# Optimization experiments

Measured on AMD Instinct MI355X. Metric: run time of the kernel, lower is better.

## Reference

```python
import jax, jax.numpy as jnp
import numpy as np

T, D, E, K, F = 512, 2048, 64, 8, 768  # tokens, hidden, experts, top_k, moe_intermediate

def setup_inputs() -> dict:
    key = jax.random.key(0)
    k0, k1, k2, k3, k4 = jax.random.split(key, 5)
    std = 0.02
    return {
        "hidden_states": jax.random.normal(k0, (T, D), dtype=jnp.float32),
        "gate_w": jax.random.normal(k1, (D, E), dtype=jnp.float32) * std,
        "w_gate": jax.random.normal(k2, (E, D, F), dtype=jnp.float32) * std,  # per-expert gate proj
        "w_up":   jax.random.normal(k3, (E, D, F), dtype=jnp.float32) * std,  # per-expert up proj
        "w_down": jax.random.normal(k4, (E, F, D), dtype=jnp.float32) * std,  # per-expert down proj
    }

def reference(hidden_states, gate_w, w_gate, w_up, w_down):
    x = hidden_states  # [T, D]
    # Router: gate linear -> softmax -> top-k -> renormalize (norm_topk_prob=True)
    router_logits = x @ gate_w                      # [T, E]
    probs = jax.nn.softmax(router_logits, axis=-1)  # [T, E]
    topk_w, topk_idx = jax.lax.top_k(probs, K)      # [T, K]
    topk_w = topk_w / jnp.sum(topk_w, axis=-1, keepdims=True)
    # Combine weights as dense [T, E] scatter (zero for unrouted experts)
    cw = jnp.zeros((T, E), dtype=x.dtype).at[jnp.arange(T)[:, None], topk_idx].set(topk_w)
    # Experts: SwiGLU MLP per expert, dense dispatch then weighted combine
    g = jnp.einsum('td,edf->etf', x, w_gate)        # [E, T, F]
    u = jnp.einsum('td,edf->etf', x, w_up)          # [E, T, F]
    h = jax.nn.silu(g) * u                          # [E, T, F]
    y = jnp.einsum('etf,efd->etd', h, w_down)       # [E, T, D]
    out = jnp.einsum('te,etd->td', cw, y)           # [T, D]
    return out
```

## Files before the change

### kernel.cpp

```cpp
#include <hip/hip_runtime.h>
#include <hip/hip_bf16.h>

#define T_TOK 512
#define D_DIM 2048
#define E_NUM 64
#define K_TOP 8
#define F_DIM 768

typedef __bf16 bf16x8 __attribute__((ext_vector_type(8)));
typedef float  f32x4  __attribute__((ext_vector_type(4)));

#define AS1 __attribute__((address_space(1)))
#define AS3 __attribute__((address_space(3)))

__device__ __forceinline__ void gll16(const void* g, void* l) {
    __builtin_amdgcn_global_load_lds((const AS1 uint32_t*)g, (AS3 uint32_t*)l, 16, 0, 0);
}

#define VM_WAIT_I(N) asm volatile("s_waitcnt vmcnt(" #N ")" ::: "memory")
#define VM_WAIT(N) VM_WAIT_I(N)

#define PIPE_STEP(WN, BUF, DOSTG, KN)            \
    do {                                          \
        VM_WAIT(WN);                              \
        __builtin_amdgcn_sched_barrier(0);        \
        __builtin_amdgcn_s_barrier();             \
        consume(BUF);                             \
        __builtin_amdgcn_s_barrier();             \
        __builtin_amdgcn_sched_barrier(0);        \
        if (DOSTG) stage(BUF, KN);                \
    } while (0)

#define WS_IDS   4096
#define WS_PW    139264
#define WS_XBF   155648
#define WS_H     2252800
#define WS_Y     8544256

__global__ void zero_cnt_kernel(int* __restrict__ cnt) {
    if (threadIdx.x < E_NUM) cnt[threadIdx.x] = 0;
}

__global__ __launch_bounds__(256) void xcvt_kernel(
        const float* __restrict__ x, __bf16* __restrict__ xb) {
    const size_t i = ((size_t)blockIdx.x * 256 + threadIdx.x) * 8;
    const float4 a = *(const float4*)(x + i);
    const float4 b = *(const float4*)(x + i + 4);
    bf16x8 v;
    v[0]=(__bf16)a.x; v[1]=(__bf16)a.y; v[2]=(__bf16)a.z; v[3]=(__bf16)a.w;
    v[4]=(__bf16)b.x; v[5]=(__bf16)b.y; v[6]=(__bf16)b.z; v[7]=(__bf16)b.w;
    *(uint4*)(xb + i) = __builtin_bit_cast(uint4, v);
}

__global__ __launch_bounds__(256) void router_kernel(
        const float* __restrict__ x, const float* __restrict__ gw,
        float* __restrict__ pair_w, int* __restrict__ cnt, int* __restrict__ ids) {
    const int t   = blockIdx.x;
    const int tid = threadIdx.x;
    const int c   = tid >> 4;
    const int g   = tid & 15;

    const float* xr  = x + (size_t)t * D_DIM + c * 128;
    const float4* gr = (const float4*)(gw + (size_t)(c * 128) * E_NUM + g * 4);

    f32x4 acc; acc[0]=0.f; acc[1]=0.f; acc[2]=0.f; acc[3]=0.f;
    #pragma unroll 8
    for (int k = 0; k < 128; k++) {
        const float xv = xr[k];
        const float4 wv = gr[(size_t)k * 16];
        acc[0] += xv * wv.x; acc[1] += xv * wv.y;
        acc[2] += xv * wv.z; acc[3] += xv * wv.w;
    }
    __shared__ f32x4 part[16][16];
    part[c][g] = acc;
    __syncthreads();
    if (tid < 64) {
        const int e = tid;
        float logit = 0.f;
        #pragma unroll
        for (int cc = 0; cc < 16; cc++) logit += part[cc][e >> 2][e & 3];
        float cur = logit;
        float selV[8]; int selE[8];
        #pragma unroll
        for (int i = 0; i < 8; i++) {
            float bv = cur; int bi = e;
            #pragma unroll
            for (int off = 32; off > 0; off >>= 1) {
                float ov = __shfl_xor(bv, off);
                int   oi = __shfl_xor(bi, off);
                if (ov > bv || (ov == bv && oi < bi)) { bv = ov; bi = oi; }
            }
            selV[i] = bv; selE[i] = bi;
            if (e == bi) cur = -INFINITY;
        }
        const float m = selV[0];
        float sum = 0.f;
        #pragma unroll
        for (int i = 0; i < 8; i++) sum += __expf(selV[i] - m);
        float myW = 0.f; int myE = 0;
        #pragma unroll
        for (int i = 0; i < 8; i++) {
            if (e == i) { myW = __expf(selV[i] - m) / sum; myE = selE[i]; }
        }
        if (e < 8) {
            pair_w[t * K_TOP + e] = myW;
            int pos = atomicAdd(&cnt[myE], 1);
            ids[myE * T_TOK + pos] = t * K_TOP + e;
        }
    }
}

template<int NK, int BSTR, int MODE>
__global__ __launch_bounds__(256, 3) void gemm2_kernel(
        const __bf16* __restrict__ Abase, const float* __restrict__ B0w,
        const float* __restrict__ B1w, const int* __restrict__ cnt,
        const int* __restrict__ ids, __bf16* __restrict__ Out) {
    constexpr int NCT = (MODE == 0) ? (BSTR / 64) : (BSTR / 128);
    constexpr int NWG = NCT * E_NUM;
    constexpr int CHK = NWG / 8;
    const int bid = blockIdx.y * NCT + blockIdx.x;
    const int wg  = (bid & 7) * CHK + (bid >> 3);
    const int e   = wg / NCT;
    const int ct  = wg % NCT;
    const int n = cnt[e];
    if (n <= 0) return;

    const int tid  = threadIdx.x;
    const int lane = tid & 63;
    const int w    = tid >> 6;
    const int g16  = lane >> 4;
    const int l16  = lane & 15;

    __shared__ __align__(16) char lds[2][24576];

    const int bcol0 = (MODE == 0) ? ct * 64 : ct * 128;
    const int bcol1 = (MODE == 0) ? ct * 64 : ct * 128 + 64;
    const float* b0 = B0w + (size_t)e * NK * 32 * BSTR
                    + (size_t)(tid >> 4) * BSTR + bcol0 + (tid & 15) * 4;
    const float* b1 = B1w + (size_t)e * NK * 32 * BSTR
                    + (size_t)(tid >> 4) * BSTR + bcol1 + (tid & 15) * 4;
    const int ach = tid >> 7;
    const int arw = tid & 127;
    const int ci  = w * 16 + l16;

    for (int mt = 0; mt * 128 < n; mt++) {
        const int ap  = mt * 128 + arw;
        const int aid = ids[(size_t)e * T_TOK + (ap < n ? ap : n - 1)];
        const __bf16* asrc = Abase + (size_t)(MODE == 0 ? (aid >> 3) : aid)
                                   * (MODE == 0 ? D_DIM : F_DIM);

        f32x4 acc0[8], acc1[8];
        #pragma unroll
        for (int m = 0; m < 8; m++) {
            acc0[m][0]=0.f; acc0[m][1]=0.f; acc0[m][2]=0.f; acc0[m][3]=0.f;
            acc1[m][0]=0.f; acc1[m][1]=0.f; acc1[m][2]=0.f; acc1[m][3]=0.f;
        }

        auto stage = [&](int buf, int ks) {
            char* L = lds[buf];
            gll16(asrc + ks * 32 + ach * 8,        L + ach * 2048 + arw * 16);
            gll16(asrc + ks * 32 + (ach + 2) * 8,  L + (ach + 2) * 2048 + arw * 16);
            gll16(b0 + (size_t)(ks * 32) * BSTR,      L + 8192 + tid * 16);
            gll16(b0 + (size_t)(ks * 32 + 16) * BSTR, L + 8192 + 4096 + tid * 16);
            gll16(b1 + (size_t)(ks * 32) * BSTR,      L + 16384 + tid * 16);
            gll16(b1 + (size_t)(ks * 32 + 16) * BSTR, L + 16384 + 4096 + tid * 16);
        };
        auto consume = [&](int buf) {
            const char* L = lds[buf];
            const float* B0f = (const float*)(L + 8192);
            const float* B1f = (const float*)(L + 16384);
            bf16x8 bf0, bf1;
            #pragma unroll
            for (int i = 0; i < 8; i++) {
                bf0[i] = (__bf16)B0f[(g16 * 8 + i) * 64 + ci];
                bf1[i] = (__bf16)B1f[(g16 * 8 + i) * 64 + ci];
            }
            __builtin_amdgcn_s_setprio(1);
            #pragma unroll
            for (int m = 0; m < 8; m++) {
                bf16x8 af = __builtin_bit_cast(bf16x8,
                    *(const uint4*)(L + g16 * 2048 + (m * 16 + l16) * 16));
                acc0[m] = __builtin_amdgcn_mfma_f32_16x16x32_bf16(af, bf0, acc0[m], 0, 0, 0);
                acc1[m] = __builtin_amdgcn_mfma_f32_16x16x32_bf16(af, bf1, acc1[m], 0, 0, 0);
            }
            __builtin_amdgcn_s_setprio(0);
        };

        stage(0, 0); stage(1, 1);

        for (int ks = 0; ks < NK - 2; ks++) {
            PIPE_STEP(6, ks & 1, true, ks + 2);
        }
        PIPE_STEP(6, NK & 1, false, 0);
        PIPE_STEP(0, (NK - 1) & 1, false, 0);

        #pragma unroll
        for (int m = 0; m < 8; m++) {
            #pragma unroll
            for (int r = 0; r < 4; r++) {
                const int p = mt * 128 + m * 16 + g16 * 4 + r;
                if (p < n) {
                    const int rid = ids[(size_t)e * T_TOK + p];
                    if (MODE == 0) {
                        const float g = acc0[m][r], u = acc1[m][r];
                        const float hv = (g / (1.f + __expf(-g))) * u;
                        Out[(size_t)rid * F_DIM + ct * 64 + ci] = (__bf16)hv;
                    } else {
                        Out[(size_t)rid * D_DIM + ct * 128 + ci]      = (__bf16)acc0[m][r];
                        Out[(size_t)rid * D_DIM + ct * 128 + 64 + ci] = (__bf16)acc1[m][r];
                    }
                }
            }
        }
    }
}

__global__ __launch_bounds__(256) void combine_kernel(
        const __bf16* __restrict__ Y, const float* __restrict__ pw,
        float* __restrict__ out) {
    const int t   = blockIdx.x;
    const int tid = threadIdx.x;
    const int d0  = tid * 8;
    float acc[8];
    #pragma unroll
    for (int j = 0; j < 8; j++) acc[j] = 0.f;
    #pragma unroll
    for (int k = 0; k < K_TOP; k++) {
        const float wgt = pw[t * K_TOP + k];
        bf16x8 v = *(const bf16x8*)(Y + (size_t)(t * K_TOP + k) * D_DIM + d0);
        #pragma unroll
        for (int j = 0; j < 8; j++) acc[j] += wgt * (float)v[j];
    }
    #pragma unroll
    for (int j = 0; j < 8; j++) out[(size_t)t * D_DIM + d0 + j] = acc[j];
}

extern "C" void kernel_launch(void* const* d_in, const int* in_sizes, int n_in,
                              void* d_out, int out_size, void* d_ws, size_t ws_size,
                              hipStream_t stream) {
    const float* x      = (const float*)d_in[0];
    const float* gw     = (const float*)d_in[1];
    const float* w_gate = (const float*)d_in[2];
    const float* w_up   = (const float*)d_in[3];
    const float* w_down = (const float*)d_in[4];
    float* out = (float*)d_out;

    char* ws = (char*)d_ws;
    int*    cnt = (int*)(ws);
    int*    ids = (int*)(ws + WS_IDS);
    float*  pw  = (float*)(ws + WS_PW);
    __bf16* xbf = (__bf16*)(ws + WS_XBF);
    __bf16* H   = (__bf16*)(ws + WS_H);
    __bf16* Y   = (__bf16*)(ws + WS_Y);

    zero_cnt_kernel<<<1, 64, 0, stream>>>(cnt);
    xcvt_kernel<<<T_TOK * D_DIM / (256 * 8), 256, 0, stream>>>(x, xbf);
    router_kernel<<<T_TOK, 256, 0, stream>>>(x, gw, pw, cnt, ids);
    gemm2_kernel<64, F_DIM, 0><<<dim3(F_DIM / 64, E_NUM), 256, 0, stream>>>(
        xbf, w_gate, w_up, cnt, ids, H);
    gemm2_kernel<24, D_DIM, 1><<<dim3(D_DIM / 128, E_NUM), 256, 0, stream>>>(
        H, w_down, w_down, cnt, ids, Y);
    combine_kernel<<<T_TOK, 256, 0, stream>>>(Y, pw, out);
}
```

Measured before the change: 303.8 us.

## Load gathered A rows directly to registers and triple-buffer B tiles in LDS

The gathered activation (A) operand is no longer staged through LDS. Each lane loads its MFMA A fragment straight from global memory into registers, with two register sets alternating across k-steps. The B weight tiles now use three LDS buffers of 16 KB each instead of two of 24 KB, so each block allocates less LDS and prefetches one step further ahead. This is meant to hide memory latency better and cut LDS traffic, at the cost of more VGPRs and uncoalesced 16-byte global gathers per lane.

```diff
diff --git a/kernel.cpp b/kernel.cpp
--- a/kernel.cpp
+++ b/kernel.cpp
@@ -19,17 +19,8 @@
 
 #define VM_WAIT_I(N) asm volatile("s_waitcnt vmcnt(" #N ")" ::: "memory")
 #define VM_WAIT(N) VM_WAIT_I(N)
-
-#define PIPE_STEP(WN, BUF, DOSTG, KN)            \
-    do {                                          \
-        VM_WAIT(WN);                              \
-        __builtin_amdgcn_sched_barrier(0);        \
-        __builtin_amdgcn_s_barrier();             \
-        consume(BUF);                             \
-        __builtin_amdgcn_s_barrier();             \
-        __builtin_amdgcn_sched_barrier(0);        \
-        if (DOSTG) stage(BUF, KN);                \
-    } while (0)
+#define SB0() __builtin_amdgcn_sched_barrier(0)
+#define BAR() __builtin_amdgcn_s_barrier()
 
 #define WS_IDS   4096
 #define WS_PW    139264
@@ -112,10 +103,11 @@
 
 template<int NK, int BSTR, int MODE>
 __global__ __launch_bounds__(256, 3) void gemm2_kernel(
-        const __bf16* __restrict__ Abase, const float* __restrict__ B0w,
+        const char* __restrict__ Abase, const float* __restrict__ B0w,
         const float* __restrict__ B1w, const int* __restrict__ cnt,
         const int* __restrict__ ids, __bf16* __restrict__ Out) {
-    constexpr int NCT = (MODE == 0) ? (BSTR / 64) : (BSTR / 128);
+    constexpr int NCT   = (MODE == 0) ? (BSTR / 64) : (BSTR / 128);
+    constexpr int ASTRB = (MODE == 0) ? (D_DIM * 2) : (F_DIM * 2);
     constexpr int NWG = NCT * E_NUM;
     constexpr int CHK = NWG / 8;
     const int bid = blockIdx.y * NCT + blockIdx.x;
@@ -131,7 +123,7 @@
     const int g16  = lane >> 4;
     const int l16  = lane & 15;
 
-    __shared__ __align__(16) char lds[2][24576];
+    __shared__ __align__(16) char lds[3][16384];
 
     const int bcol0 = (MODE == 0) ? ct * 64 : ct * 128;
     const int bcol1 = (MODE == 0) ? ct * 64 : ct * 128 + 64;
@@ -139,15 +131,18 @@
                     + (size_t)(tid >> 4) * BSTR + bcol0 + (tid & 15) * 4;
     const float* b1 = B1w + (size_t)e * NK * 32 * BSTR
                     + (size_t)(tid >> 4) * BSTR + bcol1 + (tid & 15) * 4;
-    const int ach = tid >> 7;
-    const int arw = tid & 127;
-    const int ci  = w * 16 + l16;
+    const int ci = w * 16 + l16;
 
     for (int mt = 0; mt * 128 < n; mt++) {
-        const int ap  = mt * 128 + arw;
-        const int aid = ids[(size_t)e * T_TOK + (ap < n ? ap : n - 1)];
-        const __bf16* asrc = Abase + (size_t)(MODE == 0 ? (aid >> 3) : aid)
-                                   * (MODE == 0 ? D_DIM : F_DIM);
+        uint32_t aoff[8];
+        #pragma unroll
+        for (int m = 0; m < 8; m++) {
+            int p = mt * 128 + m * 16 + l16;
+            if (p >= n) p = n - 1;
+            const int aid = ids[(size_t)e * T_TOK + p];
+            const int row = (MODE == 0) ? (aid >> 3) : aid;
+            aoff[m] = (uint32_t)row * ASTRB + g16 * 16;
+        }
 
         f32x4 acc0[8], acc1[8];
         #pragma unroll
@@ -155,20 +150,24 @@
             acc0[m][0]=0.f; acc0[m][1]=0.f; acc0[m][2]=0.f; acc0[m][3]=0.f;
             acc1[m][0]=0.f; acc1[m][1]=0.f; acc1[m][2]=0.f; acc1[m][3]=0.f;
         }
+        uint4 sA[8], sB[8];
 
         auto stage = [&](int buf, int ks) {
             char* L = lds[buf];
-            gll16(asrc + ks * 32 + ach * 8,        L + ach * 2048 + arw * 16);
-            gll16(asrc + ks * 32 + (ach + 2) * 8,  L + (ach + 2) * 2048 + arw * 16);
-            gll16(b0 + (size_t)(ks * 32) * BSTR,      L + 8192 + tid * 16);
-            gll16(b0 + (size_t)(ks * 32 + 16) * BSTR, L + 8192 + 4096 + tid * 16);
-            gll16(b1 + (size_t)(ks * 32) * BSTR,      L + 16384 + tid * 16);
-            gll16(b1 + (size_t)(ks * 32 + 16) * BSTR, L + 16384 + 4096 + tid * 16);
+            gll16(b0 + (size_t)(ks * 32) * BSTR,      L + tid * 16);
+            gll16(b0 + (size_t)(ks * 32 + 16) * BSTR, L + 4096 + tid * 16);
+            gll16(b1 + (size_t)(ks * 32) * BSTR,      L + 8192 + tid * 16);
+            gll16(b1 + (size_t)(ks * 32 + 16) * BSTR, L + 12288 + tid * 16);
         };
-        auto consume = [&](int buf) {
+        auto loadA = [&](uint4 (&s)[8], int ks) {
+            #pragma unroll
+            for (int m = 0; m < 8; m++)
+                s[m] = *(const uint4*)(Abase + aoff[m] + ks * 64);
+        };
+        auto consume = [&](int buf, const uint4 (&s)[8]) {
             const char* L = lds[buf];
-            const float* B0f = (const float*)(L + 8192);
-            const float* B1f = (const float*)(L + 16384);
+            const float* B0f = (const float*)L;
+            const float* B1f = (const float*)(L + 8192);
             bf16x8 bf0, bf1;
             #pragma unroll
             for (int i = 0; i < 8; i++) {
@@ -178,21 +177,44 @@
             __builtin_amdgcn_s_setprio(1);
             #pragma unroll
             for (int m = 0; m < 8; m++) {
-                bf16x8 af = __builtin_bit_cast(bf16x8,
-                    *(const uint4*)(L + g16 * 2048 + (m * 16 + l16) * 16));
+                const bf16x8 af = __builtin_bit_cast(bf16x8, s[m]);
                 acc0[m] = __builtin_amdgcn_mfma_f32_16x16x32_bf16(af, bf0, acc0[m], 0, 0, 0);
                 acc1[m] = __builtin_amdgcn_mfma_f32_16x16x32_bf16(af, bf1, acc1[m], 0, 0, 0);
             }
             __builtin_amdgcn_s_setprio(0);
         };
 
-        stage(0, 0); stage(1, 1);
-
-        for (int ks = 0; ks < NK - 2; ks++) {
-            PIPE_STEP(6, ks & 1, true, ks + 2);
-        }
-        PIPE_STEP(6, NK & 1, false, 0);
-        PIPE_STEP(0, (NK - 1) & 1, false, 0);
+        stage(0, 0); loadA(sA, 0);
+        stage(1, 1); loadA(sB, 1);
+        stage(2, 2);
+
+        VM_WAIT(16); SB0(); BAR();
+        consume(0, sA);
+        BAR(); SB0();
+        loadA(sA, 2); stage(0, 3);
+
+        for (int k = 1; k <= NK - 5; k += 2) {
+            VM_WAIT(16); SB0(); BAR();
+            consume(k % 3, sB);
+            BAR(); SB0();
+            loadA(sB, k + 2); stage(k % 3, k + 3);
+
+            VM_WAIT(16); SB0(); BAR();
+            consume((k + 1) % 3, sA);
+            BAR(); SB0();
+            loadA(sA, k + 3); stage((k + 1) % 3, k + 4);
+        }
+
+        VM_WAIT(16); SB0(); BAR();
+        consume((NK - 3) % 3, sB);
+        BAR(); SB0();
+        loadA(sB, NK - 1);
+        VM_WAIT(12); SB0(); BAR();
+        consume((NK - 2) % 3, sA);
+        BAR(); SB0();
+        VM_WAIT(0); SB0(); BAR();
+        consume((NK - 1) % 3, sB);
+        BAR(); SB0();
 
         #pragma unroll
         for (int m = 0; m < 8; m++) {
@@ -257,8 +279,8 @@
     xcvt_kernel<<<T_TOK * D_DIM / (256 * 8), 256, 0, stream>>>(x, xbf);
     router_kernel<<<T_TOK, 256, 0, stream>>>(x, gw, pw, cnt, ids);
     gemm2_kernel<64, F_DIM, 0><<<dim3(F_DIM / 64, E_NUM), 256, 0, stream>>>(
-        xbf, w_gate, w_up, cnt, ids, H);
+        (const char*)xbf, w_gate, w_up, cnt, ids, H);
     gemm2_kernel<24, D_DIM, 1><<<dim3(D_DIM / 128, E_NUM), 256, 0, stream>>>(
-        H, w_down, w_down, cnt, ids, Y);
+        (const char*)H, w_down, w_down, cnt, ids, Y);
     combine_kernel<<<T_TOK, 256, 0, stream>>>(Y, pw, out);
 }
```

Result: slower. 576.4 us (+89.7%).

## Split GEMM consume into two halves interleaved with staging, fuse bf16 cast into router

Applied to the files above, without the earlier changes.

The x-to-bf16 conversion moves into the router kernel, removing one launch and a separate pass over x. In the expert GEMMs, each k-step now runs in two halves (gate/B0, then up/B1) with A fragments held in registers. Loads for the next stage are issued between the halves, so memory traffic overlaps with MFMA work instead of waiting for the whole consume to finish. This adds an extra barrier per step and more register pressure from holding the A fragments.

```diff
diff --git a/kernel.cpp b/kernel.cpp
--- a/kernel.cpp
+++ b/kernel.cpp
@@ -19,17 +19,8 @@
 
 #define VM_WAIT_I(N) asm volatile("s_waitcnt vmcnt(" #N ")" ::: "memory")
 #define VM_WAIT(N) VM_WAIT_I(N)
-
-#define PIPE_STEP(WN, BUF, DOSTG, KN)            \
-    do {                                          \
-        VM_WAIT(WN);                              \
-        __builtin_amdgcn_sched_barrier(0);        \
-        __builtin_amdgcn_s_barrier();             \
-        consume(BUF);                             \
-        __builtin_amdgcn_s_barrier();             \
-        __builtin_amdgcn_sched_barrier(0);        \
-        if (DOSTG) stage(BUF, KN);                \
-    } while (0)
+#define SB0() __builtin_amdgcn_sched_barrier(0)
+#define BAR() __builtin_amdgcn_s_barrier()
 
 #define WS_IDS   4096
 #define WS_PW    139264
@@ -41,20 +32,10 @@
     if (threadIdx.x < E_NUM) cnt[threadIdx.x] = 0;
 }
 
-__global__ __launch_bounds__(256) void xcvt_kernel(
-        const float* __restrict__ x, __bf16* __restrict__ xb) {
-    const size_t i = ((size_t)blockIdx.x * 256 + threadIdx.x) * 8;
-    const float4 a = *(const float4*)(x + i);
-    const float4 b = *(const float4*)(x + i + 4);
-    bf16x8 v;
-    v[0]=(__bf16)a.x; v[1]=(__bf16)a.y; v[2]=(__bf16)a.z; v[3]=(__bf16)a.w;
-    v[4]=(__bf16)b.x; v[5]=(__bf16)b.y; v[6]=(__bf16)b.z; v[7]=(__bf16)b.w;
-    *(uint4*)(xb + i) = __builtin_bit_cast(uint4, v);
-}
-
 __global__ __launch_bounds__(256) void router_kernel(
         const float* __restrict__ x, const float* __restrict__ gw,
-        float* __restrict__ pair_w, int* __restrict__ cnt, int* __restrict__ ids) {
+        float* __restrict__ pair_w, int* __restrict__ cnt, int* __restrict__ ids,
+        __bf16* __restrict__ xb) {
     const int t   = blockIdx.x;
     const int tid = threadIdx.x;
     const int c   = tid >> 4;
@@ -71,6 +52,15 @@
         acc[0] += xv * wv.x; acc[1] += xv * wv.y;
         acc[2] += xv * wv.z; acc[3] += xv * wv.w;
     }
+    {
+        const size_t i = (size_t)t * D_DIM + tid * 8;
+        const float4 a = *(const float4*)(x + i);
+        const float4 b = *(const float4*)(x + i + 4);
+        bf16x8 v;
+        v[0]=(__bf16)a.x; v[1]=(__bf16)a.y; v[2]=(__bf16)a.z; v[3]=(__bf16)a.w;
+        v[4]=(__bf16)b.x; v[5]=(__bf16)b.y; v[6]=(__bf16)b.z; v[7]=(__bf16)b.w;
+        *(uint4*)(xb + i) = __builtin_bit_cast(uint4, v);
+    }
     __shared__ f32x4 part[16][16];
     part[c][g] = acc;
     __syncthreads();
@@ -112,10 +102,11 @@
 
 template<int NK, int BSTR, int MODE>
 __global__ __launch_bounds__(256, 3) void gemm2_kernel(
-        const __bf16* __restrict__ Abase, const float* __restrict__ B0w,
+        const char* __restrict__ Abase, const float* __restrict__ B0w,
         const float* __restrict__ B1w, const int* __restrict__ cnt,
         const int* __restrict__ ids, __bf16* __restrict__ Out) {
-    constexpr int NCT = (MODE == 0) ? (BSTR / 64) : (BSTR / 128);
+    constexpr int NCT   = (MODE == 0) ? (BSTR / 64) : (BSTR / 128);
+    constexpr int ASTRB = (MODE == 0) ? (D_DIM * 2) : (F_DIM * 2);
     constexpr int NWG = NCT * E_NUM;
     constexpr int CHK = NWG / 8;
     const int bid = blockIdx.y * NCT + blockIdx.x;
@@ -146,8 +137,7 @@
     for (int mt = 0; mt * 128 < n; mt++) {
         const int ap  = mt * 128 + arw;
         const int aid = ids[(size_t)e * T_TOK + (ap < n ? ap : n - 1)];
-        const __bf16* asrc = Abase + (size_t)(MODE == 0 ? (aid >> 3) : aid)
-                                   * (MODE == 0 ? D_DIM : F_DIM);
+        const char* asrc = Abase + (size_t)(MODE == 0 ? (aid >> 3) : aid) * ASTRB;
 
         f32x4 acc0[8], acc1[8];
         #pragma unroll
@@ -156,43 +146,72 @@
             acc1[m][0]=0.f; acc1[m][1]=0.f; acc1[m][2]=0.f; acc1[m][3]=0.f;
         }
 
-        auto stage = [&](int buf, int ks) {
+        auto stageB0 = [&](int buf, int ks) {
             char* L = lds[buf];
-            gll16(asrc + ks * 32 + ach * 8,        L + ach * 2048 + arw * 16);
-            gll16(asrc + ks * 32 + (ach + 2) * 8,  L + (ach + 2) * 2048 + arw * 16);
             gll16(b0 + (size_t)(ks * 32) * BSTR,      L + 8192 + tid * 16);
-            gll16(b0 + (size_t)(ks * 32 + 16) * BSTR, L + 8192 + 4096 + tid * 16);
+            gll16(b0 + (size_t)(ks * 32 + 16) * BSTR, L + 12288 + tid * 16);
+        };
+        auto stageAB1 = [&](int buf, int ks) {
+            char* L = lds[buf];
+            gll16(asrc + ks * 64 + ach * 16,        L + ach * 2048 + arw * 16);
+            gll16(asrc + ks * 64 + (ach + 2) * 16,  L + (ach + 2) * 2048 + arw * 16);
             gll16(b1 + (size_t)(ks * 32) * BSTR,      L + 16384 + tid * 16);
-            gll16(b1 + (size_t)(ks * 32 + 16) * BSTR, L + 16384 + 4096 + tid * 16);
-        };
-        auto consume = [&](int buf) {
+            gll16(b1 + (size_t)(ks * 32 + 16) * BSTR, L + 20480 + tid * 16);
+        };
+        auto half0 = [&](int buf, uint4 (&af)[8]) {
             const char* L = lds[buf];
             const float* B0f = (const float*)(L + 8192);
+            bf16x8 bf0;
+            #pragma unroll
+            for (int i = 0; i < 8; i++) bf0[i] = (__bf16)B0f[(g16 * 8 + i) * 64 + ci];
+            #pragma unroll
+            for (int m = 0; m < 8; m++)
+                af[m] = *(const uint4*)(L + g16 * 2048 + (m * 16 + l16) * 16);
+            __builtin_amdgcn_s_setprio(1);
+            #pragma unroll
+            for (int m = 0; m < 8; m++)
+                acc0[m] = __builtin_amdgcn_mfma_f32_16x16x32_bf16(
+                    __builtin_bit_cast(bf16x8, af[m]), bf0, acc0[m], 0, 0, 0);
+            __builtin_amdgcn_s_setprio(0);
+        };
+        auto half1 = [&](int buf, const uint4 (&af)[8]) {
+            const char* L = lds[buf];
             const float* B1f = (const float*)(L + 16384);
-            bf16x8 bf0, bf1;
-            #pragma unroll
-            for (int i = 0; i < 8; i++) {
-                bf0[i] = (__bf16)B0f[(g16 * 8 + i) * 64 + ci];
-                bf1[i] = (__bf16)B1f[(g16 * 8 + i) * 64 + ci];
-            }
+            bf16x8 bf1;
+            #pragma unroll
+            for (int i = 0; i < 8; i++) bf1[i] = (__bf16)B1f[(g16 * 8 + i) * 64 + ci];
             __builtin_amdgcn_s_setprio(1);
             #pragma unroll
-            for (int m = 0; m < 8; m++) {
-                bf16x8 af = __builtin_bit_cast(bf16x8,
-                    *(const uint4*)(L + g16 * 2048 + (m * 16 + l16) * 16));
-                acc0[m] = __builtin_amdgcn_mfma_f32_16x16x32_bf16(af, bf0, acc0[m], 0, 0, 0);
-                acc1[m] = __builtin_amdgcn_mfma_f32_16x16x32_bf16(af, bf1, acc1[m], 0, 0, 0);
-            }
+            for (int m = 0; m < 8; m++)
+                acc1[m] = __builtin_amdgcn_mfma_f32_16x16x32_bf16(
+                    __builtin_bit_cast(bf16x8, af[m]), bf1, acc1[m], 0, 0, 0);
             __builtin_amdgcn_s_setprio(0);
         };
 
-        stage(0, 0); stage(1, 1);
-
+        stageB0(0, 0); stageAB1(0, 0);
+        stageB0(1, 1); stageAB1(1, 1);
+
+        uint4 af[8];
         for (int ks = 0; ks < NK - 2; ks++) {
-            PIPE_STEP(6, ks & 1, true, ks + 2);
-        }
-        PIPE_STEP(6, NK & 1, false, 0);
-        PIPE_STEP(0, (NK - 1) & 1, false, 0);
+            const int buf = ks & 1;
+            VM_WAIT(6); SB0(); BAR();
+            half0(buf, af);
+            BAR(); SB0();
+            stageB0(buf, ks + 2);
+            half1(buf, af);
+            BAR(); SB0();
+            stageAB1(buf, ks + 2);
+        }
+        VM_WAIT(6); SB0(); BAR();
+        half0(NK & 1, af);
+        BAR(); SB0();
+        half1(NK & 1, af);
+        BAR(); SB0();
+        VM_WAIT(0); SB0(); BAR();
+        half0((NK - 1) & 1, af);
+        BAR(); SB0();
+        half1((NK - 1) & 1, af);
+        BAR(); SB0();
 
         #pragma unroll
         for (int m = 0; m < 8; m++) {
@@ -254,11 +273,10 @@
     __bf16* Y   = (__bf16*)(ws + WS_Y);
 
     zero_cnt_kernel<<<1, 64, 0, stream>>>(cnt);
-    xcvt_kernel<<<T_TOK * D_DIM / (256 * 8), 256, 0, stream>>>(x, xbf);
-    router_kernel<<<T_TOK, 256, 0, stream>>>(x, gw, pw, cnt, ids);
+    router_kernel<<<T_TOK, 256, 0, stream>>>(x, gw, pw, cnt, ids, xbf);
     gemm2_kernel<64, F_DIM, 0><<<dim3(F_DIM / 64, E_NUM), 256, 0, stream>>>(
-        xbf, w_gate, w_up, cnt, ids, H);
+        (const char*)xbf, w_gate, w_up, cnt, ids, H);
     gemm2_kernel<24, D_DIM, 1><<<dim3(D_DIM / 128, E_NUM), 256, 0, stream>>>(
-        H, w_down, w_down, cnt, ids, Y);
+        (const char*)H, w_down, w_down, cnt, ids, Y);
     combine_kernel<<<T_TOK, 256, 0, stream>>>(Y, pw, out);
 }
```

After: 316.6 us. 4.2% more time.

## Fuse x-conversion into router, batch 8 tokens per router block, widen down-proj tile

Applied to the files above, without the earlier changes.

The router now handles 8 tokens per block so each gate-weight load is reused across tokens, and it also writes the bf16 copy of x, which removes the separate conversion kernel. The down-projection gets its own kernel with a 256-column tile (4 column groups per wave), so each A tile in LDS serves more MFMAs and fewer workgroups re-read the same token rows. The cost is larger LDS (80KB) and more accumulators, which lowers occupancy to 2 blocks per CU. The router grid also shrinks to 64 blocks, which may underfill the GPU.

```diff
diff --git a/kernel.cpp b/kernel.cpp
--- a/kernel.cpp
+++ b/kernel.cpp
@@ -41,83 +41,101 @@
     if (threadIdx.x < E_NUM) cnt[threadIdx.x] = 0;
 }
 
-__global__ __launch_bounds__(256) void xcvt_kernel(
-        const float* __restrict__ x, __bf16* __restrict__ xb) {
-    const size_t i = ((size_t)blockIdx.x * 256 + threadIdx.x) * 8;
-    const float4 a = *(const float4*)(x + i);
-    const float4 b = *(const float4*)(x + i + 4);
-    bf16x8 v;
-    v[0]=(__bf16)a.x; v[1]=(__bf16)a.y; v[2]=(__bf16)a.z; v[3]=(__bf16)a.w;
-    v[4]=(__bf16)b.x; v[5]=(__bf16)b.y; v[6]=(__bf16)b.z; v[7]=(__bf16)b.w;
-    *(uint4*)(xb + i) = __builtin_bit_cast(uint4, v);
-}
-
 __global__ __launch_bounds__(256) void router_kernel(
         const float* __restrict__ x, const float* __restrict__ gw,
-        float* __restrict__ pair_w, int* __restrict__ cnt, int* __restrict__ ids) {
-    const int t   = blockIdx.x;
+        float* __restrict__ pair_w, int* __restrict__ cnt, int* __restrict__ ids,
+        __bf16* __restrict__ xb) {
+    const int t0  = blockIdx.x * 8;
     const int tid = threadIdx.x;
     const int c   = tid >> 4;
     const int g   = tid & 15;
 
-    const float* xr  = x + (size_t)t * D_DIM + c * 128;
+    const float*  xr = x + (size_t)t0 * D_DIM + c * 128;
     const float4* gr = (const float4*)(gw + (size_t)(c * 128) * E_NUM + g * 4);
 
-    f32x4 acc; acc[0]=0.f; acc[1]=0.f; acc[2]=0.f; acc[3]=0.f;
-    #pragma unroll 8
-    for (int k = 0; k < 128; k++) {
-        const float xv = xr[k];
-        const float4 wv = gr[(size_t)k * 16];
-        acc[0] += xv * wv.x; acc[1] += xv * wv.y;
-        acc[2] += xv * wv.z; acc[3] += xv * wv.w;
-    }
-    __shared__ f32x4 part[16][16];
-    part[c][g] = acc;
+    f32x4 acc[8];
+    #pragma unroll
+    for (int t = 0; t < 8; t++) { acc[t][0]=0.f; acc[t][1]=0.f; acc[t][2]=0.f; acc[t][3]=0.f; }
+
+    for (int k4 = 0; k4 < 32; k4++) {
+        float4 wv[4];
+        #pragma unroll
+        for (int j = 0; j < 4; j++) wv[j] = gr[(size_t)(k4 * 4 + j) * 16];
+        #pragma unroll
+        for (int t = 0; t < 8; t++) {
+            const float4 xq = *(const float4*)(xr + t * D_DIM + k4 * 4);
+            acc[t][0] += xq.x*wv[0].x + xq.y*wv[1].x + xq.z*wv[2].x + xq.w*wv[3].x;
+            acc[t][1] += xq.x*wv[0].y + xq.y*wv[1].y + xq.z*wv[2].y + xq.w*wv[3].y;
+            acc[t][2] += xq.x*wv[0].z + xq.y*wv[1].z + xq.z*wv[2].z + xq.w*wv[3].z;
+            acc[t][3] += xq.x*wv[0].w + xq.y*wv[1].w + xq.z*wv[2].w + xq.w*wv[3].w;
+        }
+    }
+
+    {
+        const float* xsrc = x  + (size_t)t0 * D_DIM;
+        __bf16*      xd   = xb + (size_t)t0 * D_DIM;
+        #pragma unroll
+        for (int j = 0; j < 8; j++) {
+            const int o = (j * 256 + tid) * 8;
+            const float4 a = *(const float4*)(xsrc + o);
+            const float4 b = *(const float4*)(xsrc + o + 4);
+            bf16x8 v;
+            v[0]=(__bf16)a.x; v[1]=(__bf16)a.y; v[2]=(__bf16)a.z; v[3]=(__bf16)a.w;
+            v[4]=(__bf16)b.x; v[5]=(__bf16)b.y; v[6]=(__bf16)b.z; v[7]=(__bf16)b.w;
+            *(uint4*)(xd + o) = __builtin_bit_cast(uint4, v);
+        }
+    }
+
+    __shared__ f32x4 part[8][16][16];
+    #pragma unroll
+    for (int t = 0; t < 8; t++) part[t][c][g] = acc[t];
     __syncthreads();
+
     if (tid < 64) {
         const int e = tid;
-        float logit = 0.f;
-        #pragma unroll
-        for (int cc = 0; cc < 16; cc++) logit += part[cc][e >> 2][e & 3];
-        float cur = logit;
-        float selV[8]; int selE[8];
-        #pragma unroll
-        for (int i = 0; i < 8; i++) {
-            float bv = cur; int bi = e;
-            #pragma unroll
-            for (int off = 32; off > 0; off >>= 1) {
-                float ov = __shfl_xor(bv, off);
-                int   oi = __shfl_xor(bi, off);
-                if (ov > bv || (ov == bv && oi < bi)) { bv = ov; bi = oi; }
-            }
-            selV[i] = bv; selE[i] = bi;
-            if (e == bi) cur = -INFINITY;
-        }
-        const float m = selV[0];
-        float sum = 0.f;
-        #pragma unroll
-        for (int i = 0; i < 8; i++) sum += __expf(selV[i] - m);
-        float myW = 0.f; int myE = 0;
-        #pragma unroll
-        for (int i = 0; i < 8; i++) {
-            if (e == i) { myW = __expf(selV[i] - m) / sum; myE = selE[i]; }
-        }
-        if (e < 8) {
-            pair_w[t * K_TOP + e] = myW;
-            int pos = atomicAdd(&cnt[myE], 1);
-            ids[myE * T_TOK + pos] = t * K_TOP + e;
-        }
-    }
-}
-
-template<int NK, int BSTR, int MODE>
-__global__ __launch_bounds__(256, 3) void gemm2_kernel(
+        for (int t = 0; t < 8; t++) {
+            float logit = 0.f;
+            #pragma unroll
+            for (int cc = 0; cc < 16; cc++) logit += part[t][cc][e >> 2][e & 3];
+            float cur = logit;
+            float selV[8]; int selE[8];
+            #pragma unroll
+            for (int i = 0; i < 8; i++) {
+                float bv = cur; int bi = e;
+                #pragma unroll
+                for (int off = 32; off > 0; off >>= 1) {
+                    float ov = __shfl_xor(bv, off);
+                    int   oi = __shfl_xor(bi, off);
+                    if (ov > bv || (ov == bv && oi < bi)) { bv = ov; bi = oi; }
+                }
+                selV[i] = bv; selE[i] = bi;
+                if (e == bi) cur = -INFINITY;
+            }
+            const float m = selV[0];
+            float sum = 0.f;
+            #pragma unroll
+            for (int i = 0; i < 8; i++) sum += __expf(selV[i] - m);
+            float myW = 0.f; int myE = 0;
+            #pragma unroll
+            for (int i = 0; i < 8; i++) {
+                if (e == i) { myW = __expf(selV[i] - m) / sum; myE = selE[i]; }
+            }
+            if (e < 8) {
+                pair_w[(t0 + t) * K_TOP + e] = myW;
+                int pos = atomicAdd(&cnt[myE], 1);
+                ids[myE * T_TOK + pos] = (t0 + t) * K_TOP + e;
+            }
+        }
+    }
+}
+
+__global__ __launch_bounds__(256, 3) void gemm_gu_kernel(
         const __bf16* __restrict__ Abase, const float* __restrict__ B0w,
         const float* __restrict__ B1w, const int* __restrict__ cnt,
         const int* __restrict__ ids, __bf16* __restrict__ Out) {
-    constexpr int NCT = (MODE == 0) ? (BSTR / 64) : (BSTR / 128);
-    constexpr int NWG = NCT * E_NUM;
-    constexpr int CHK = NWG / 8;
+    constexpr int NK  = 64;
+    constexpr int NCT = F_DIM / 64;
+    constexpr int CHK = NCT * E_NUM / 8;
     const int bid = blockIdx.y * NCT + blockIdx.x;
     const int wg  = (bid & 7) * CHK + (bid >> 3);
     const int e   = wg / NCT;
@@ -133,21 +151,19 @@
 
     __shared__ __align__(16) char lds[2][24576];
 
-    const int bcol0 = (MODE == 0) ? ct * 64 : ct * 128;
-    const int bcol1 = (MODE == 0) ? ct * 64 : ct * 128 + 64;
-    const float* b0 = B0w + (size_t)e * NK * 32 * BSTR
-                    + (size_t)(tid >> 4) * BSTR + bcol0 + (tid & 15) * 4;
-    const float* b1 = B1w + (size_t)e * NK * 32 * BSTR
-                    + (size_t)(tid >> 4) * BSTR + bcol1 + (tid & 15) * 4;
+    const float* b0 = B0w + (size_t)e * D_DIM * F_DIM
+                    + (size_t)(tid >> 4) * F_DIM + ct * 64 + (tid & 15) * 4;
+    const float* b1 = B1w + (size_t)e * D_DIM * F_DIM
+                    + (size_t)(tid >> 4) * F_DIM + ct * 64 + (tid & 15) * 4;
     const int ach = tid >> 7;
     const int arw = tid & 127;
     const int ci  = w * 16 + l16;
 
     for (int mt = 0; mt * 128 < n; mt++) {
+        __builtin_amdgcn_s_barrier();
         const int ap  = mt * 128 + arw;
         const int aid = ids[(size_t)e * T_TOK + (ap < n ? ap : n - 1)];
-        const __bf16* asrc = Abase + (size_t)(MODE == 0 ? (aid >> 3) : aid)
-                                   * (MODE == 0 ? D_DIM : F_DIM);
+        const __bf16* asrc = Abase + (size_t)(aid >> 3) * D_DIM;
 
         f32x4 acc0[8], acc1[8];
         #pragma unroll
@@ -158,12 +174,12 @@
 
         auto stage = [&](int buf, int ks) {
             char* L = lds[buf];
-            gll16(asrc + ks * 32 + ach * 8,        L + ach * 2048 + arw * 16);
-            gll16(asrc + ks * 32 + (ach + 2) * 8,  L + (ach + 2) * 2048 + arw * 16);
-            gll16(b0 + (size_t)(ks * 32) * BSTR,      L + 8192 + tid * 16);
-            gll16(b0 + (size_t)(ks * 32 + 16) * BSTR, L + 8192 + 4096 + tid * 16);
-            gll16(b1 + (size_t)(ks * 32) * BSTR,      L + 16384 + tid * 16);
-            gll16(b1 + (size_t)(ks * 32 + 16) * BSTR, L + 16384 + 4096 + tid * 16);
+            gll16(asrc + ks * 32 + ach * 8,           L + ach * 2048 + arw * 16);
+            gll16(asrc + ks * 32 + (ach + 2) * 8,     L + (ach + 2) * 2048 + arw * 16);
+            gll16(b0 + (size_t)(ks * 32) * F_DIM,      L + 8192 + tid * 16);
+            gll16(b0 + (size_t)(ks * 32 + 16) * F_DIM, L + 12288 + tid * 16);
+            gll16(b1 + (size_t)(ks * 32) * F_DIM,      L + 16384 + tid * 16);
+            gll16(b1 + (size_t)(ks * 32 + 16) * F_DIM, L + 20480 + tid * 16);
         };
         auto consume = [&](int buf) {
             const char* L = lds[buf];
@@ -187,7 +203,6 @@
         };
 
         stage(0, 0); stage(1, 1);
-
         for (int ks = 0; ks < NK - 2; ks++) {
             PIPE_STEP(6, ks & 1, true, ks + 2);
         }
@@ -201,14 +216,106 @@
                 const int p = mt * 128 + m * 16 + g16 * 4 + r;
                 if (p < n) {
                     const int rid = ids[(size_t)e * T_TOK + p];
-                    if (MODE == 0) {
-                        const float g = acc0[m][r], u = acc1[m][r];
-                        const float hv = (g / (1.f + __expf(-g))) * u;
-                        Out[(size_t)rid * F_DIM + ct * 64 + ci] = (__bf16)hv;
-                    } else {
-                        Out[(size_t)rid * D_DIM + ct * 128 + ci]      = (__bf16)acc0[m][r];
-                        Out[(size_t)rid * D_DIM + ct * 128 + 64 + ci] = (__bf16)acc1[m][r];
-                    }
+                    const float g = acc0[m][r], u = acc1[m][r];
+                    const float hv = (g / (1.f + __expf(-g))) * u;
+                    Out[(size_t)rid * F_DIM + ct * 64 + ci] = (__bf16)hv;
+                }
+            }
+        }
+    }
+}
+
+__global__ __launch_bounds__(256, 2) void gemm_down_kernel(
+        const __bf16* __restrict__ Abase, const float* __restrict__ Bw,
+        const int* __restrict__ cnt, const int* __restrict__ ids,
+        __bf16* __restrict__ Out) {
+    constexpr int NK  = 24;
+    constexpr int NCT = D_DIM / 256;
+    constexpr int CHK = NCT * E_NUM / 8;
+    const int bid = blockIdx.y * NCT + blockIdx.x;
+    const int wg  = (bid & 7) * CHK + (bid >> 3);
+    const int e   = wg / NCT;
+    const int ct  = wg % NCT;
+    const int n = cnt[e];
+    if (n <= 0) return;
+
+    const int tid  = threadIdx.x;
+    const int lane = tid & 63;
+    const int w    = tid >> 6;
+    const int g16  = lane >> 4;
+    const int l16  = lane & 15;
+
+    __shared__ __align__(16) char lds[2][40960];
+
+    const float* bsrc = Bw + (size_t)e * F_DIM * D_DIM
+                      + (size_t)(tid >> 6) * D_DIM + ct * 256 + (tid & 63) * 4;
+    const int ach = tid >> 7;
+    const int arw = tid & 127;
+
+    for (int mt = 0; mt * 128 < n; mt++) {
+        __builtin_amdgcn_s_barrier();
+        const int ap  = mt * 128 + arw;
+        const int aid = ids[(size_t)e * T_TOK + (ap < n ? ap : n - 1)];
+        const __bf16* asrc = Abase + (size_t)aid * F_DIM;
+
+        f32x4 acc[4][8];
+        #pragma unroll
+        for (int cg = 0; cg < 4; cg++)
+            #pragma unroll
+            for (int m = 0; m < 8; m++) {
+                acc[cg][m][0]=0.f; acc[cg][m][1]=0.f;
+                acc[cg][m][2]=0.f; acc[cg][m][3]=0.f;
+            }
+
+        auto stage = [&](int buf, int ks) {
+            char* L = lds[buf];
+            gll16(asrc + ks * 32 + ach * 8,       L + ach * 2048 + arw * 16);
+            gll16(asrc + ks * 32 + (ach + 2) * 8, L + (ach + 2) * 2048 + arw * 16);
+            #pragma unroll
+            for (int j = 0; j < 8; j++)
+                gll16(bsrc + (size_t)(ks * 32 + j * 4) * D_DIM,
+                      L + 8192 + j * 4096 + tid * 16);
+        };
+        auto consume = [&](int buf) {
+            const char* L = lds[buf];
+            const float* Bf = (const float*)(L + 8192);
+            uint4 af[8];
+            #pragma unroll
+            for (int m = 0; m < 8; m++)
+                af[m] = *(const uint4*)(L + g16 * 2048 + (m * 16 + l16) * 16);
+            #pragma unroll
+            for (int cg = 0; cg < 4; cg++) {
+                bf16x8 bf;
+                #pragma unroll
+                for (int i = 0; i < 8; i++)
+                    bf[i] = (__bf16)Bf[(g16 * 8 + i) * 256 + cg * 64 + w * 16 + l16];
+                __builtin_amdgcn_s_setprio(1);
+                #pragma unroll
+                for (int m = 0; m < 8; m++)
+                    acc[cg][m] = __builtin_amdgcn_mfma_f32_16x16x32_bf16(
+                        __builtin_bit_cast(bf16x8, af[m]), bf, acc[cg][m], 0, 0, 0);
+                __builtin_amdgcn_s_setprio(0);
+            }
+        };
+
+        stage(0, 0); stage(1, 1);
+        for (int ks = 0; ks < NK - 2; ks++) {
+            PIPE_STEP(10, ks & 1, true, ks + 2);
+        }
+        PIPE_STEP(10, NK & 1, false, 0);
+        PIPE_STEP(0, (NK - 1) & 1, false, 0);
+
+        #pragma unroll
+        for (int m = 0; m < 8; m++) {
+            #pragma unroll
+            for (int r = 0; r < 4; r++) {
+                const int p = mt * 128 + m * 16 + g16 * 4 + r;
+                if (p < n) {
+                    const int rid = ids[(size_t)e * T_TOK + p];
+                    const size_t base = (size_t)rid * D_DIM + ct * 256 + w * 16 + l16;
+                    #pragma unroll
+                    for (int cg = 0; cg < 4; cg++)
+                        Out[base + cg * 64] = (__bf16)acc[cg][m][r];
                 }
             }
         }
@@ -254,11 +361,10 @@
     __bf16* Y   = (__bf16*)(ws + WS_Y);
 
     zero_cnt_kernel<<<1, 64, 0, stream>>>(cnt);
-    xcvt_kernel<<<T_TOK * D_DIM / (256 * 8), 256, 0, stream>>>(x, xbf);
-    router_kernel<<<T_TOK, 256, 0, stream>>>(x, gw, pw, cnt, ids);
-    gemm2_kernel<64, F_DIM, 0><<<dim3(F_DIM / 64, E_NUM), 256, 0, stream>>>(
+    router_kernel<<<T_TOK / 8, 256, 0, stream>>>(x, gw, pw, cnt, ids, xbf);
+    gemm_gu_kernel<<<dim3(F_DIM / 64, E_NUM), 256, 0, stream>>>(
         xbf, w_gate, w_up, cnt, ids, H);
-    gemm2_kernel<24, D_DIM, 1><<<dim3(D_DIM / 128, E_NUM), 256, 0, stream>>>(
-        H, w_down, w_down, cnt, ids, Y);
+    gemm_down_kernel<<<dim3(D_DIM / 256, E_NUM), 256, 0, stream>>>(
+        H, w_down, cnt, ids, Y);
     combine_kernel<<<T_TOK, 256, 0, stream>>>(Y, pw, out);
 }
```

Result: slower. 329.7 us (+8.5%).
